# Optimization experiments

Hardware: AMD Instinct MI355X
Metric: run time of the kernel (lower is better)

The kernel has to match this reference:

```python
import jax, jax.numpy as jnp
import numpy as np

B, N, K, D = 2, 50000, 16, 64
EPS = 1e-5

def _ln(x, s, b):
    m = jnp.mean(x, axis=-1, keepdims=True)
    v = jnp.var(x, axis=-1, keepdims=True)
    return (x - m) * jax.lax.rsqrt(v + EPS) * s + b

def _lrelu(x):
    return jnp.where(x >= 0, x, 0.2 * x)

def _mlp3(x, w1, b1, ls1, lb1, w2, b2, ls2, lb2, w3, b3):
    h = _lrelu(_ln(jnp.dot(x, w1) + b1, ls1, lb1))
    h = _lrelu(_ln(jnp.dot(h, w2) + b2, ls2, lb2))
    return jnp.dot(h, w3) + b3

def _lin_init(k, fan_in, fan_out):
    bound = 1.0 / np.sqrt(fan_in)
    kw, kb = jax.random.split(k)
    w = jax.random.uniform(kw, (fan_in, fan_out), jnp.float32, -bound, bound)
    b = jax.random.uniform(kb, (fan_out,), jnp.float32, -bound, bound)
    return w, b

def setup_inputs() -> dict:
    key = jax.random.key(0)
    ks = jax.random.split(key, 10)
    inp = {
        'point_features': jax.random.normal(ks[0], (B, N, D), jnp.float32),
        'geom_features': jax.random.normal(ks[1], (B, N, K, 4), jnp.float32),
        'neighbor_idxs': jax.random.randint(ks[2], (B, N, K), 0, N, jnp.int32),
    }
    # geom_mlp: 4 -> 64 -> 128 -> 64 (Linear+LN+LeakyReLU x2, final Linear)
    inp['g_w1'], inp['g_b1'] = _lin_init(ks[3], 4, 64)
    inp['g_ls1'] = jnp.ones((64,), jnp.float32); inp['g_lb1'] = jnp.zeros((64,), jnp.float32)
    inp['g_w2'], inp['g_b2'] = _lin_init(ks[4], 64, 128)
    inp['g_ls2'] = jnp.ones((128,), jnp.float32); inp['g_lb2'] = jnp.zeros((128,), jnp.float32)
    inp['g_w3'], inp['g_b3'] = _lin_init(ks[5], 128, D)
    # feature_mlp: 2*D=128 -> 64 -> 128 -> 64
    inp['f_w1'], inp['f_b1'] = _lin_init(ks[6], 2 * D, 64)
    inp['f_ls1'] = jnp.ones((64,), jnp.float32); inp['f_lb1'] = jnp.zeros((64,), jnp.float32)
    inp['f_w2'], inp['f_b2'] = _lin_init(ks[7], 64, 128)
    inp['f_ls2'] = jnp.ones((128,), jnp.float32); inp['f_lb2'] = jnp.zeros((128,), jnp.float32)
    inp['f_w3'], inp['f_b3'] = _lin_init(ks[8], 128, D)
    return inp

def reference(point_features, geom_features, neighbor_idxs,
              g_w1, g_b1, g_ls1, g_lb1, g_w2, g_b2, g_ls2, g_lb2, g_w3, g_b3,
              f_w1, f_b1, f_ls1, f_lb1, f_w2, f_b2, f_ls2, f_lb2, f_w3, f_b3):
    b, n, k = neighbor_idxs.shape
    c = point_features.shape[-1]
    # geometry MLP on (B,N,K,4)
    geom_out = _mlp3(geom_features, g_w1, g_b1, g_ls1, g_lb1,
                     g_w2, g_b2, g_ls2, g_lb2, g_w3, g_b3)  # (B,N,K,D)
    # gather: out[b,i,j,:] = point_features[b, neighbor_idxs[b,i,j], :]
    gathered = jnp.take_along_axis(
        point_features, neighbor_idxs.reshape(b, n * k)[:, :, None], axis=1
    ).reshape(b, n, k, c)
    combined = jnp.concatenate([geom_out, gathered], axis=-1)  # (B,N,K,2D)
    final = _mlp3(combined, f_w1, f_b1, f_ls1, f_lb1,
                  f_w2, f_b2, f_ls2, f_lb2, f_w3, f_b3)  # (B,N,K,D)
    return jnp.mean(final, axis=2)  # (B,N,D)
```

## Files before the change

kernel.cpp:

```cpp
#include <hip/hip_runtime.h>
#include <hip/hip_bf16.h>

#define NN 50000
#define TB 512
#define NBLK 256
#define WPB 8
#define STR (NBLK * WPB)
static constexpr float EPS = 1e-5f;

typedef __attribute__((ext_vector_type(8))) short short8;
typedef __attribute__((ext_vector_type(16))) float f32x16;
typedef unsigned int u32;

#define OFF_G2 0
#define OFF_G3 16
#define OFF_F1 32
#define OFF_F2 48
#define OFF_W3 64
#define NFRAGS 80

__device__ __forceinline__ u32 pkbf(float a, float b) {
  u32 lo = (u32)__builtin_bit_cast(unsigned short, __float2bfloat16(a));
  u32 hi = (u32)__builtin_bit_cast(unsigned short, __float2bfloat16(b));
  return lo | (hi << 16);
}
__device__ __forceinline__ f32x16 zero16() {
  f32x16 z;
#pragma unroll
  for (int i = 0; i < 16; ++i) z[i] = 0.f;
  return z;
}
#define MFMA __builtin_amdgcn_mfma_f32_32x32x16_bf16

template <int IN, int OUT>
__device__ __forceinline__ void stage(const float* __restrict__ W,
                                      uint4* __restrict__ lds, int fragoff,
                                      float scale, int tid) {
  constexpr int KS = IN / 16, MT = OUT / 32;
  constexpr int ENT = MT * KS * 64;
  for (int e = tid; e < ENT; e += TB) {
    int lane = e & 63, f = e >> 6;
    int mt = f / KS, ks = f - mt * KS;
    int h = lane >> 5, och = mt * 32 + (lane & 31);
    int k0 = ks * 16 + h * 8;
    u32 d[4];
#pragma unroll
    for (int p = 0; p < 4; ++p)
      d[p] = pkbf(W[(k0 + 2 * p) * OUT + och] * scale,
                  W[(k0 + 2 * p + 1) * OUT + och] * scale);
    lds[(fragoff + f) * 64 + lane] = make_uint4(d[0], d[1], d[2], d[3]);
  }
}

__device__ __forceinline__ short8 rdfrag(const uint4* __restrict__ lds,
                                         int fragidx, int lane) {
  return __builtin_bit_cast(short8, lds[fragidx * 64 + lane]);
}

template <int NK>
__device__ __forceinline__ void to_bfr(const f32x16* acc, short8* bfr) {
#pragma unroll
  for (int t = 0; t < NK; ++t) {
    const int mt = t >> 1, q0 = (t & 1) * 8;
    u32 P0 = pkbf(acc[mt][q0 + 0], acc[mt][q0 + 1]);
    u32 P1 = pkbf(acc[mt][q0 + 2], acc[mt][q0 + 3]);
    u32 P2 = pkbf(acc[mt][q0 + 4], acc[mt][q0 + 5]);
    u32 P3 = pkbf(acc[mt][q0 + 6], acc[mt][q0 + 7]);
    auto s1 = __builtin_amdgcn_permlane32_swap((int)P0, (int)P2, false, false);
    auto s2 = __builtin_amdgcn_permlane32_swap((int)P1, (int)P3, false, false);
    bfr[t] = __builtin_bit_cast(
        short8, make_uint4((u32)s1[0], (u32)s2[0], (u32)s1[1], (u32)s2[1]));
  }
}

__device__ __forceinline__ void add_bias64_dual(f32x16* A, f32x16* B,
                                                const float* __restrict__ bias,
                                                int lane) {
  const int h = (lane >> 5) & 1;
#pragma unroll
  for (int mt = 0; mt < 2; ++mt)
#pragma unroll
    for (int rq = 0; rq < 4; ++rq) {
      const float4 b4 = *(const float4*)(bias + 32 * mt + 8 * rq + 4 * h);
      const float bb[4] = {b4.x, b4.y, b4.z, b4.w};
#pragma unroll
      for (int c = 0; c < 4; ++c) {
        A[mt][4 * rq + c] += bb[c];
        B[mt][4 * rq + c] += bb[c];
      }
    }
}

__device__ __forceinline__ void bias_ln_act64_dual(
    f32x16* A, f32x16* B, const float* __restrict__ bias,
    const float* __restrict__ gam, const float* __restrict__ bet, int lane) {
  const int h = (lane >> 5) & 1;
  float sA = 0.f, qA = 0.f, sB = 0.f, qB = 0.f;
#pragma unroll
  for (int mt = 0; mt < 2; ++mt)
#pragma unroll
    for (int rq = 0; rq < 4; ++rq) {
      const float4 b4 = *(const float4*)(bias + 32 * mt + 8 * rq + 4 * h);
      const float bb[4] = {b4.x, b4.y, b4.z, b4.w};
#pragma unroll
      for (int c = 0; c < 4; ++c) {
        float va = A[mt][4 * rq + c] + bb[c];
        float vb = B[mt][4 * rq + c] + bb[c];
        A[mt][4 * rq + c] = va;
        B[mt][4 * rq + c] = vb;
        sA += va; qA += va * va;
        sB += vb; qB += vb * vb;
      }
    }
  sA += __shfl_xor(sA, 32); qA += __shfl_xor(qA, 32);
  sB += __shfl_xor(sB, 32); qB += __shfl_xor(qB, 32);
  const float mA = sA * (1.f / 64.f);
  const float iA = rsqrtf(qA * (1.f / 64.f) - mA * mA + EPS);
  const float mB = sB * (1.f / 64.f);
  const float iB = rsqrtf(qB * (1.f / 64.f) - mB * mB + EPS);
#pragma unroll
  for (int mt = 0; mt < 2; ++mt)
#pragma unroll
    for (int rq = 0; rq < 4; ++rq) {
      const float4 g4 = *(const float4*)(gam + 32 * mt + 8 * rq + 4 * h);
      const float4 c4 = *(const float4*)(bet + 32 * mt + 8 * rq + 4 * h);
      const float gg[4] = {g4.x, g4.y, g4.z, g4.w};
      const float cc[4] = {c4.x, c4.y, c4.z, c4.w};
#pragma unroll
      for (int c = 0; c < 4; ++c) {
        float ya = (A[mt][4 * rq + c] - mA) * iA * gg[c] + cc[c];
        float yb = (B[mt][4 * rq + c] - mB) * iB * gg[c] + cc[c];
        A[mt][4 * rq + c] = fmaxf(ya, 0.2f * ya);
        B[mt][4 * rq + c] = fmaxf(yb, 0.2f * yb);
      }
    }
}

__device__ __forceinline__ void fused128_dual(
    const short8* kinA, const short8* kinB, const float* __restrict__ bias,
    const float* __restrict__ gam, const float* __restrict__ bet,
    const uint4* __restrict__ lds, int inOff, int outOff, f32x16* outA,
    f32x16* outB, int lane) {
  const int h = (lane >> 5) & 1;
  float sA = 0.f, qA = 0.f, sB = 0.f, qB = 0.f;
#pragma unroll 1
  for (int mt = 0; mt < 4; ++mt) {
    f32x16 a = zero16(), b = zero16();
#pragma unroll
    for (int ks = 0; ks < 4; ++ks) {
      const short8 wf = rdfrag(lds, inOff + mt * 4 + ks, lane);
      a = MFMA(wf, kinA[ks], a, 0, 0, 0);
      b = MFMA(wf, kinB[ks], b, 0, 0, 0);
    }
#pragma unroll
    for (int rq = 0; rq < 4; ++rq) {
      const float4 b4 = *(const float4*)(bias + 32 * mt + 8 * rq + 4 * h);
      const float bb[4] = {b4.x, b4.y, b4.z, b4.w};
#pragma unroll
      for (int c = 0; c < 4; ++c) {
        float va = a[4 * rq + c] + bb[c];
        float vb = b[4 * rq + c] + bb[c];
        sA += va; qA += va * va;
        sB += vb; qB += vb * vb;
      }
    }
  }
  sA += __shfl_xor(sA, 32); qA += __shfl_xor(qA, 32);
  sB += __shfl_xor(sB, 32); qB += __shfl_xor(qB, 32);
  const float mA = sA * (1.f / 128.f);
  const float iA = rsqrtf(qA * (1.f / 128.f) - mA * mA + EPS);
  const float mB = sB * (1.f / 128.f);
  const float iB = rsqrtf(qB * (1.f / 128.f) - mB * mB + EPS);
  asm volatile("" ::: "memory");
  outA[0] = zero16(); outA[1] = zero16();
  outB[0] = zero16(); outB[1] = zero16();
#pragma unroll 1
  for (int mt = 0; mt < 4; ++mt) {
    f32x16 a = zero16(), b = zero16();
#pragma unroll
    for (int ks = 0; ks < 4; ++ks) {
      const short8 wf = rdfrag(lds, inOff + mt * 4 + ks, lane);
      a = MFMA(wf, kinA[ks], a, 0, 0, 0);
      b = MFMA(wf, kinB[ks], b, 0, 0, 0);
    }
#pragma unroll
    for (int u = 0; u < 2; ++u) {
      const int c0 = 32 * mt + 16 * u + 4 * h;
      const float4 ba4 = *(const float4*)(bias + c0);
      const float4 bb4 = *(const float4*)(bias + c0 + 8);
      const float4 ga4 = *(const float4*)(gam + c0);
      const float4 gb4 = *(const float4*)(gam + c0 + 8);
      const float4 ca4 = *(const float4*)(bet + c0);
      const float4 cb4 = *(const float4*)(bet + c0 + 8);
      const float BB[8] = {ba4.x, ba4.y, ba4.z, ba4.w, bb4.x, bb4.y, bb4.z, bb4.w};
      const float GG[8] = {ga4.x, ga4.y, ga4.z, ga4.w, gb4.x, gb4.y, gb4.z, gb4.w};
      const float CC[8] = {ca4.x, ca4.y, ca4.z, ca4.w, cb4.x, cb4.y, cb4.z, cb4.w};
      u32 PA[4], PB[4];
#pragma unroll
      for (int p = 0; p < 4; ++p) {
        float a0 = (a[8 * u + 2 * p] + BB[2 * p] - mA) * iA * GG[2 * p] + CC[2 * p];
        float a1 = (a[8 * u + 2 * p + 1] + BB[2 * p + 1] - mA) * iA * GG[2 * p + 1] + CC[2 * p + 1];
        float b0 = (b[8 * u + 2 * p] + BB[2 * p] - mB) * iB * GG[2 * p] + CC[2 * p];
        float b1 = (b[8 * u + 2 * p + 1] + BB[2 * p + 1] - mB) * iB * GG[2 * p + 1] + CC[2 * p + 1];
        a0 = fmaxf(a0, 0.2f * a0); a1 = fmaxf(a1, 0.2f * a1);
        b0 = fmaxf(b0, 0.2f * b0); b1 = fmaxf(b1, 0.2f * b1);
        PA[p] = pkbf(a0, a1);
        PB[p] = pkbf(b0, b1);
      }
      auto sa1 = __builtin_amdgcn_permlane32_swap((int)PA[0], (int)PA[2], false, false);
      auto sa2 = __builtin_amdgcn_permlane32_swap((int)PA[1], (int)PA[3], false, false);
      auto sb1 = __builtin_amdgcn_permlane32_swap((int)PB[0], (int)PB[2], false, false);
      auto sb2 = __builtin_amdgcn_permlane32_swap((int)PB[1], (int)PB[3], false, false);
      const short8 frA = __builtin_bit_cast(
          short8, make_uint4((u32)sa1[0], (u32)sa2[0], (u32)sa1[1], (u32)sa2[1]));
      const short8 frB = __builtin_bit_cast(
          short8, make_uint4((u32)sb1[0], (u32)sb2[0], (u32)sb1[1], (u32)sb2[1]));
      const int t = 2 * mt + u;
      const short8 w0 = rdfrag(lds, outOff + t, lane);
      const short8 w1 = rdfrag(lds, outOff + 8 + t, lane);
      outA[0] = MFMA(w0, frA, outA[0], 0, 0, 0);
      outA[1] = MFMA(w1, frA, outA[1], 0, 0, 0);
      outB[0] = MFMA(w0, frB, outB[0], 0, 0, 0);
      outB[1] = MFMA(w1, frB, outB[1], 0, 0, 0);
    }
  }
}

extern "C" __global__ void __launch_bounds__(TB)
    __attribute__((amdgpu_waves_per_eu(2, 2)))
lfa_mfma(const float* __restrict__ pf, const float* __restrict__ geom,
         const int* __restrict__ nidx,
         const float* __restrict__ g_w1, const float* __restrict__ g_b1,
         const float* __restrict__ g_ls1, const float* __restrict__ g_lb1,
         const float* __restrict__ g_w2, const float* __restrict__ g_b2,
         const float* __restrict__ g_ls2, const float* __restrict__ g_lb2,
         const float* __restrict__ g_w3, const float* __restrict__ g_b3,
         const float* __restrict__ f_w1, const float* __restrict__ f_b1,
         const float* __restrict__ f_ls1, const float* __restrict__ f_lb1,
         const float* __restrict__ f_w2, const float* __restrict__ f_b2,
         const float* __restrict__ f_ls2, const float* __restrict__ f_lb2,
         const float* __restrict__ f_w3, const float* __restrict__ f_b3,
         float* __restrict__ out) {
  extern __shared__ uint4 lds[];
  const int tid = threadIdx.x;

  stage<64, 128>(g_w2, lds, OFF_G2, 1.f, tid);
  stage<128, 64>(g_w3, lds, OFF_G3, 1.f, tid);
  stage<128, 64>(f_w1, lds, OFF_F1, 1.f, tid);
  stage<64, 128>(f_w2, lds, OFF_F2, 1.f, tid);
  stage<128, 64>(f_w3, lds, OFF_W3, 1.f / 16.f, tid);
  __syncthreads();

  const int lane = tid & 63;
  const int w = tid >> 6;
  const int h = lane >> 5;
  const int p31 = lane & 31;

  short8 a1[2];
#pragma unroll
  for (int mt = 0; mt < 2; ++mt) {
    const int och = 32 * mt + p31;
    uint4 qq;
    qq.x = h ? 0u : pkbf(g_w1[0 * 64 + och], g_w1[1 * 64 + och]);
    qq.y = h ? 0u : pkbf(g_w1[2 * 64 + och], g_w1[3 * 64 + och]);
    qq.z = 0u;
    qq.w = 0u;
    a1[mt] = __builtin_bit_cast(short8, qq);
  }

  short8 kinA[4], kinB[4];

  for (int t0 = blockIdx.x * WPB + w; t0 < NN; t0 += 2 * STR) {
    asm volatile("" ::: "memory");
    const int tileA = t0;
    const bool hasB = (t0 + STR) < NN;
    const int tileB = hasB ? (t0 + STR) : tileA;
    const int rrowA = tileA * 32 + p31;
    const int rrowB = tileB * 32 + p31;
    const int bbA = tileA / 25000;
    const int bbB = tileB / 25000;

    const int idxA = nidx[rrowA];
    const int idxB = nidx[rrowB];
    const float* prA = pf + ((size_t)bbA * NN + idxA) * 64;
    const float* prB = pf + ((size_t)bbB * NN + idxB) * 64;

    const float4 gA = *(const float4*)(geom + (size_t)rrowA * 4);
    const float4 gB = *(const float4*)(geom + (size_t)rrowB * 4);
    uint4 qA, qB;
    qA.x = h ? 0u : pkbf(gA.x, gA.y);
    qA.y = h ? 0u : pkbf(gA.z, gA.w);
    qA.z = 0u; qA.w = 0u;
    qB.x = h ? 0u : pkbf(gB.x, gB.y);
    qB.y = h ? 0u : pkbf(gB.z, gB.w);
    qB.z = 0u; qB.w = 0u;
    const short8 gfA = __builtin_bit_cast(short8, qA);
    const short8 gfB = __builtin_bit_cast(short8, qB);
    f32x16 accA[2], accB[2];
#pragma unroll
    for (int mt = 0; mt < 2; ++mt) {
      accA[mt] = MFMA(a1[mt], gfA, zero16(), 0, 0, 0);
      accB[mt] = MFMA(a1[mt], gfB, zero16(), 0, 0, 0);
    }
    bias_ln_act64_dual(accA, accB, g_b1, g_ls1, g_lb1, lane);
    to_bfr<4>(accA, kinA);
    to_bfr<4>(accB, kinB);

    fused128_dual(kinA, kinB, g_b2, g_ls2, g_lb2, lds, OFF_G2, OFF_G3, accA,
                  accB, lane);
    add_bias64_dual(accA, accB, g_b3, lane);
    to_bfr<4>(accA, kinA);
    to_bfr<4>(accB, kinB);

#pragma unroll
    for (int mt = 0; mt < 2; ++mt) {
      f32x16 ta = zero16(), tb = zero16();
#pragma unroll
      for (int ks = 0; ks < 4; ++ks) {
        const short8 wf = rdfrag(lds, OFF_F1 + mt * 8 + ks, lane);
        ta = MFMA(wf, kinA[ks], ta, 0, 0, 0);
        tb = MFMA(wf, kinB[ks], tb, 0, 0, 0);
      }
      accA[mt] = ta;
      accB[mt] = tb;
    }
    {
#pragma unroll
      for (int t = 0; t < 4; ++t) {
        const float4 xA = *(const float4*)(prA + 16 * t + 8 * h);
        const float4 yA = *(const float4*)(prA + 16 * t + 8 * h + 4);
        const float4 xB = *(const float4*)(prB + 16 * t + 8 * h);
        const float4 yB = *(const float4*)(prB + 16 * t + 8 * h + 4);
        const short8 fA = __builtin_bit_cast(
            short8, make_uint4(pkbf(xA.x, xA.y), pkbf(xA.z, xA.w),
                               pkbf(yA.x, yA.y), pkbf(yA.z, yA.w)));
        const short8 fB = __builtin_bit_cast(
            short8, make_uint4(pkbf(xB.x, xB.y), pkbf(xB.z, xB.w),
                               pkbf(yB.x, yB.y), pkbf(yB.z, yB.w)));
        const short8 w0 = rdfrag(lds, OFF_F1 + 4 + t, lane);
        const short8 w1 = rdfrag(lds, OFF_F1 + 12 + t, lane);
        accA[0] = MFMA(w0, fA, accA[0], 0, 0, 0);
        accA[1] = MFMA(w1, fA, accA[1], 0, 0, 0);
        accB[0] = MFMA(w0, fB, accB[0], 0, 0, 0);
        accB[1] = MFMA(w1, fB, accB[1], 0, 0, 0);
      }
    }
    bias_ln_act64_dual(accA, accB, f_b1, f_ls1, f_lb1, lane);
    to_bfr<4>(accA, kinA);
    to_bfr<4>(accB, kinB);

    fused128_dual(kinA, kinB, f_b2, f_ls2, f_lb2, lds, OFF_F2, OFF_W3, accA,
                  accB, lane);

#pragma unroll
    for (int mt = 0; mt < 2; ++mt)
#pragma unroll
      for (int r = 0; r < 16; ++r) {
        float va = accA[mt][r];
        float vb = accB[mt][r];
        va += __shfl_xor(va, 1); vb += __shfl_xor(vb, 1);
        va += __shfl_xor(va, 2); vb += __shfl_xor(vb, 2);
        va += __shfl_xor(va, 4); vb += __shfl_xor(vb, 4);
        va += __shfl_xor(va, 8); vb += __shfl_xor(vb, 8);
        accA[mt][r] = va;
        accB[mt][r] = vb;
      }
    if ((lane & 15) < 4) {
      const int c = lane & 15;
      const int bn = (lane >> 4) & 1;
      const size_t rowA = (size_t)tileA * 2 + bn;
      const size_t rowB = (size_t)tileB * 2 + bn;
#pragma unroll
      for (int mt = 0; mt < 2; ++mt) {
        const float4 bq = *(const float4*)(f_b3 + 32 * mt + 8 * c + 4 * h);
        const float4 vA =
            (c == 0) ? make_float4(accA[mt][0], accA[mt][1], accA[mt][2], accA[mt][3])
          : (c == 1) ? make_float4(accA[mt][4], accA[mt][5], accA[mt][6], accA[mt][7])
          : (c == 2) ? make_float4(accA[mt][8], accA[mt][9], accA[mt][10], accA[mt][11])
                     : make_float4(accA[mt][12], accA[mt][13], accA[mt][14], accA[mt][15]);
        *(float4*)(out + rowA * 64 + 32 * mt + 8 * c + 4 * h) =
            make_float4(vA.x + bq.x, vA.y + bq.y, vA.z + bq.z, vA.w + bq.w);
        if (hasB) {
          const float4 vB =
              (c == 0) ? make_float4(accB[mt][0], accB[mt][1], accB[mt][2], accB[mt][3])
            : (c == 1) ? make_float4(accB[mt][4], accB[mt][5], accB[mt][6], accB[mt][7])
            : (c == 2) ? make_float4(accB[mt][8], accB[mt][9], accB[mt][10], accB[mt][11])
                       : make_float4(accB[mt][12], accB[mt][13], accB[mt][14], accB[mt][15]);
          *(float4*)(out + rowB * 64 + 32 * mt + 8 * c + 4 * h) =
              make_float4(vB.x + bq.x, vB.y + bq.y, vB.z + bq.z, vB.w + bq.w);
        }
      }
    }
  }
}

extern "C" void kernel_launch(void* const* d_in, const int* in_sizes, int n_in,
                              void* d_out, int out_size, void* d_ws, size_t ws_size,
                              hipStream_t stream) {
  const float* pf = (const float*)d_in[0];
  const float* geom = (const float*)d_in[1];
  const int* nidx = (const int*)d_in[2];
  const float* g_w1 = (const float*)d_in[3];
  const float* g_b1 = (const float*)d_in[4];
  const float* g_ls1 = (const float*)d_in[5];
  const float* g_lb1 = (const float*)d_in[6];
  const float* g_w2 = (const float*)d_in[7];
  const float* g_b2 = (const float*)d_in[8];
  const float* g_ls2 = (const float*)d_in[9];
  const float* g_lb2 = (const float*)d_in[10];
  const float* g_w3 = (const float*)d_in[11];
  const float* g_b3 = (const float*)d_in[12];
  const float* f_w1 = (const float*)d_in[13];
  const float* f_b1 = (const float*)d_in[14];
  const float* f_ls1 = (const float*)d_in[15];
  const float* f_lb1 = (const float*)d_in[16];
  const float* f_w2 = (const float*)d_in[17];
  const float* f_b2 = (const float*)d_in[18];
  const float* f_ls2 = (const float*)d_in[19];
  const float* f_lb2 = (const float*)d_in[20];
  const float* f_w3 = (const float*)d_in[21];
  const float* f_b3 = (const float*)d_in[22];

  const int shmem = NFRAGS * 64 * 16;
  lfa_mfma<<<NBLK, TB, shmem, stream>>>(
      pf, geom, nidx, g_w1, g_b1, g_ls1, g_lb1, g_w2, g_b2, g_ls2, g_lb2, g_w3,
      g_b3, f_w1, f_b1, f_ls1, f_lb1, f_w2, f_b2, f_ls2, f_lb2, f_w3, f_b3,
      (float*)d_out);
}
```

Baseline: 384.8 us.

## Switch MFMA operands to fp16 and do LayerNorm/activation in packed half math

```diff
diff --git a/kernel.cpp b/kernel.cpp
--- a/kernel.cpp
+++ b/kernel.cpp
@@ -8,7 +8,8 @@
 #define STR (NBLK * WPB)
 static constexpr float EPS = 1e-5f;
 
-typedef __attribute__((ext_vector_type(8))) short short8;
+typedef _Float16 h2 __attribute__((ext_vector_type(2)));
+typedef _Float16 half8 __attribute__((ext_vector_type(8)));
 typedef __attribute__((ext_vector_type(16))) float f32x16;
 typedef unsigned int u32;
 
@@ -19,18 +20,17 @@
 #define OFF_W3 64
 #define NFRAGS 80
 
-__device__ __forceinline__ u32 pkbf(float a, float b) {
-  u32 lo = (u32)__builtin_bit_cast(unsigned short, __float2bfloat16(a));
-  u32 hi = (u32)__builtin_bit_cast(unsigned short, __float2bfloat16(b));
-  return lo | (hi << 16);
-}
+__device__ __forceinline__ h2 pkh(float a, float b) {
+  return __builtin_bit_cast(h2, __builtin_amdgcn_cvt_pkrtz(a, b));
+}
+__device__ __forceinline__ u32 hbits(h2 x) { return __builtin_bit_cast(u32, x); }
 __device__ __forceinline__ f32x16 zero16() {
   f32x16 z;
 #pragma unroll
   for (int i = 0; i < 16; ++i) z[i] = 0.f;
   return z;
 }
-#define MFMA __builtin_amdgcn_mfma_f32_32x32x16_bf16
+#define MFMA __builtin_amdgcn_mfma_f32_32x32x16_f16
 
 template <int IN, int OUT>
 __device__ __forceinline__ void stage(const float* __restrict__ W,
@@ -46,54 +46,25 @@
     u32 d[4];
 #pragma unroll
     for (int p = 0; p < 4; ++p)
-      d[p] = pkbf(W[(k0 + 2 * p) * OUT + och] * scale,
-                  W[(k0 + 2 * p + 1) * OUT + och] * scale);
+      d[p] = hbits(pkh(W[(k0 + 2 * p) * OUT + och] * scale,
+                       W[(k0 + 2 * p + 1) * OUT + och] * scale));
     lds[(fragoff + f) * 64 + lane] = make_uint4(d[0], d[1], d[2], d[3]);
   }
 }
 
-__device__ __forceinline__ short8 rdfrag(const uint4* __restrict__ lds,
-                                         int fragidx, int lane) {
-  return __builtin_bit_cast(short8, lds[fragidx * 64 + lane]);
-}
-
-template <int NK>
-__device__ __forceinline__ void to_bfr(const f32x16* acc, short8* bfr) {
-#pragma unroll
-  for (int t = 0; t < NK; ++t) {
-    const int mt = t >> 1, q0 = (t & 1) * 8;
-    u32 P0 = pkbf(acc[mt][q0 + 0], acc[mt][q0 + 1]);
-    u32 P1 = pkbf(acc[mt][q0 + 2], acc[mt][q0 + 3]);
-    u32 P2 = pkbf(acc[mt][q0 + 4], acc[mt][q0 + 5]);
-    u32 P3 = pkbf(acc[mt][q0 + 6], acc[mt][q0 + 7]);
-    auto s1 = __builtin_amdgcn_permlane32_swap((int)P0, (int)P2, false, false);
-    auto s2 = __builtin_amdgcn_permlane32_swap((int)P1, (int)P3, false, false);
-    bfr[t] = __builtin_bit_cast(
-        short8, make_uint4((u32)s1[0], (u32)s2[0], (u32)s1[1], (u32)s2[1]));
-  }
-}
-
-__device__ __forceinline__ void add_bias64_dual(f32x16* A, f32x16* B,
-                                                const float* __restrict__ bias,
-                                                int lane) {
-  const int h = (lane >> 5) & 1;
-#pragma unroll
-  for (int mt = 0; mt < 2; ++mt)
-#pragma unroll
-    for (int rq = 0; rq < 4; ++rq) {
-      const float4 b4 = *(const float4*)(bias + 32 * mt + 8 * rq + 4 * h);
-      const float bb[4] = {b4.x, b4.y, b4.z, b4.w};
-#pragma unroll
-      for (int c = 0; c < 4; ++c) {
-        A[mt][4 * rq + c] += bb[c];
-        B[mt][4 * rq + c] += bb[c];
-      }
-    }
-}
-
-__device__ __forceinline__ void bias_ln_act64_dual(
+__device__ __forceinline__ half8 rdfrag(const uint4* __restrict__ lds,
+                                        int fragidx, int lane) {
+  return __builtin_bit_cast(half8, lds[fragidx * 64 + lane]);
+}
+
+__device__ __forceinline__ half8 mkfrag(u32 a, u32 b, u32 c, u32 d) {
+  return __builtin_bit_cast(half8, make_uint4(a, b, c, d));
+}
+
+__device__ __forceinline__ void ln_pack64_dual(
     f32x16* A, f32x16* B, const float* __restrict__ bias,
-    const float* __restrict__ gam, const float* __restrict__ bet, int lane) {
+    const float* __restrict__ gam, const float* __restrict__ bet, int lane,
+    half8* kinA, half8* kinB) {
   const int h = (lane >> 5) & 1;
   float sA = 0.f, qA = 0.f, sB = 0.f, qB = 0.f;
 #pragma unroll
@@ -118,26 +89,75 @@
   const float iA = rsqrtf(qA * (1.f / 64.f) - mA * mA + EPS);
   const float mB = sB * (1.f / 64.f);
   const float iB = rsqrtf(qB * (1.f / 64.f) - mB * mB + EPS);
+  const h2 iA2 = pkh(iA, iA), nA2 = pkh(-mA * iA, -mA * iA);
+  const h2 iB2 = pkh(iB, iB), nB2 = pkh(-mB * iB, -mB * iB);
+  const h2 c02 = pkh(0.2f, 0.2f);
 #pragma unroll
   for (int mt = 0; mt < 2; ++mt)
 #pragma unroll
-    for (int rq = 0; rq < 4; ++rq) {
-      const float4 g4 = *(const float4*)(gam + 32 * mt + 8 * rq + 4 * h);
-      const float4 c4 = *(const float4*)(bet + 32 * mt + 8 * rq + 4 * h);
-      const float gg[4] = {g4.x, g4.y, g4.z, g4.w};
-      const float cc[4] = {c4.x, c4.y, c4.z, c4.w};
-#pragma unroll
-      for (int c = 0; c < 4; ++c) {
-        float ya = (A[mt][4 * rq + c] - mA) * iA * gg[c] + cc[c];
-        float yb = (B[mt][4 * rq + c] - mB) * iB * gg[c] + cc[c];
-        A[mt][4 * rq + c] = fmaxf(ya, 0.2f * ya);
-        B[mt][4 * rq + c] = fmaxf(yb, 0.2f * yb);
-      }
+    for (int t2 = 0; t2 < 2; ++t2) {
+      const int q0 = t2 * 8;
+      const float4 g0 = *(const float4*)(gam + 32 * mt + 2 * q0 + 4 * h);
+      const float4 g1 = *(const float4*)(gam + 32 * mt + 2 * q0 + 8 + 4 * h);
+      const float4 e0 = *(const float4*)(bet + 32 * mt + 2 * q0 + 4 * h);
+      const float4 e1 = *(const float4*)(bet + 32 * mt + 2 * q0 + 8 + 4 * h);
+      const float GG[8] = {g0.x, g0.y, g0.z, g0.w, g1.x, g1.y, g1.z, g1.w};
+      const float CC[8] = {e0.x, e0.y, e0.z, e0.w, e1.x, e1.y, e1.z, e1.w};
+      u32 PA[4], PB[4];
+#pragma unroll
+      for (int p = 0; p < 4; ++p) {
+        const h2 g2 = pkh(GG[2 * p], GG[2 * p + 1]);
+        const h2 e2 = pkh(CC[2 * p], CC[2 * p + 1]);
+        h2 xa = pkh(A[mt][q0 + 2 * p], A[mt][q0 + 2 * p + 1]);
+        h2 xb = pkh(B[mt][q0 + 2 * p], B[mt][q0 + 2 * p + 1]);
+        h2 ya = (xa * iA2 + nA2) * g2 + e2;
+        h2 yb = (xb * iB2 + nB2) * g2 + e2;
+        ya = __builtin_elementwise_max(ya, ya * c02);
+        yb = __builtin_elementwise_max(yb, yb * c02);
+        PA[p] = hbits(ya);
+        PB[p] = hbits(yb);
+      }
+      auto sa1 = __builtin_amdgcn_permlane32_swap((int)PA[0], (int)PA[2], false, false);
+      auto sa2 = __builtin_amdgcn_permlane32_swap((int)PA[1], (int)PA[3], false, false);
+      auto sb1 = __builtin_amdgcn_permlane32_swap((int)PB[0], (int)PB[2], false, false);
+      auto sb2 = __builtin_amdgcn_permlane32_swap((int)PB[1], (int)PB[3], false, false);
+      kinA[2 * mt + t2] = mkfrag((u32)sa1[0], (u32)sa2[0], (u32)sa1[1], (u32)sa2[1]);
+      kinB[2 * mt + t2] = mkfrag((u32)sb1[0], (u32)sb2[0], (u32)sb1[1], (u32)sb2[1]);
+    }
+}
+
+__device__ __forceinline__ void bias_pack64_dual(const f32x16* A, const f32x16* B,
+                                                 const float* __restrict__ bias,
+                                                 int lane, half8* kinA,
+                                                 half8* kinB) {
+  const int h = (lane >> 5) & 1;
+#pragma unroll
+  for (int mt = 0; mt < 2; ++mt)
+#pragma unroll
+    for (int t2 = 0; t2 < 2; ++t2) {
+      const int q0 = t2 * 8;
+      const float4 b0 = *(const float4*)(bias + 32 * mt + 2 * q0 + 4 * h);
+      const float4 b1 = *(const float4*)(bias + 32 * mt + 2 * q0 + 8 + 4 * h);
+      const float BBv[8] = {b0.x, b0.y, b0.z, b0.w, b1.x, b1.y, b1.z, b1.w};
+      u32 PA[4], PB[4];
+#pragma unroll
+      for (int p = 0; p < 4; ++p) {
+        PA[p] = hbits(pkh(A[mt][q0 + 2 * p] + BBv[2 * p],
+                          A[mt][q0 + 2 * p + 1] + BBv[2 * p + 1]));
+        PB[p] = hbits(pkh(B[mt][q0 + 2 * p] + BBv[2 * p],
+                          B[mt][q0 + 2 * p + 1] + BBv[2 * p + 1]));
+      }
+      auto sa1 = __builtin_amdgcn_permlane32_swap((int)PA[0], (int)PA[2], false, false);
+      auto sa2 = __builtin_amdgcn_permlane32_swap((int)PA[1], (int)PA[3], false, false);
+      auto sb1 = __builtin_amdgcn_permlane32_swap((int)PB[0], (int)PB[2], false, false);
+      auto sb2 = __builtin_amdgcn_permlane32_swap((int)PB[1], (int)PB[3], false, false);
+      kinA[2 * mt + t2] = mkfrag((u32)sa1[0], (u32)sa2[0], (u32)sa1[1], (u32)sa2[1]);
+      kinB[2 * mt + t2] = mkfrag((u32)sb1[0], (u32)sb2[0], (u32)sb1[1], (u32)sb2[1]);
     }
 }
 
 __device__ __forceinline__ void fused128_dual(
-    const short8* kinA, const short8* kinB, const float* __restrict__ bias,
+    const half8* kinA, const half8* kinB, const float* __restrict__ bias,
     const float* __restrict__ gam, const float* __restrict__ bet,
     const uint4* __restrict__ lds, int inOff, int outOff, f32x16* outA,
     f32x16* outB, int lane) {
@@ -148,7 +168,7 @@
     f32x16 a = zero16(), b = zero16();
 #pragma unroll
     for (int ks = 0; ks < 4; ++ks) {
-      const short8 wf = rdfrag(lds, inOff + mt * 4 + ks, lane);
+      const half8 wf = rdfrag(lds, inOff + mt * 4 + ks, lane);
       a = MFMA(wf, kinA[ks], a, 0, 0, 0);
       b = MFMA(wf, kinB[ks], b, 0, 0, 0);
     }
@@ -171,6 +191,9 @@
   const float iA = rsqrtf(qA * (1.f / 128.f) - mA * mA + EPS);
   const float mB = sB * (1.f / 128.f);
   const float iB = rsqrtf(qB * (1.f / 128.f) - mB * mB + EPS);
+  const h2 iA2 = pkh(iA, iA), nA2 = pkh(-mA * iA, -mA * iA);
+  const h2 iB2 = pkh(iB, iB), nB2 = pkh(-mB * iB, -mB * iB);
+  const h2 c02 = pkh(0.2f, 0.2f);
   asm volatile("" ::: "memory");
   outA[0] = zero16(); outA[1] = zero16();
   outB[0] = zero16(); outB[1] = zero16();
@@ -179,7 +202,7 @@
     f32x16 a = zero16(), b = zero16();
 #pragma unroll
     for (int ks = 0; ks < 4; ++ks) {
-      const short8 wf = rdfrag(lds, inOff + mt * 4 + ks, lane);
+      const half8 wf = rdfrag(lds, inOff + mt * 4 + ks, lane);
       a = MFMA(wf, kinA[ks], a, 0, 0, 0);
       b = MFMA(wf, kinB[ks], b, 0, 0, 0);
     }
@@ -198,26 +221,26 @@
       u32 PA[4], PB[4];
 #pragma unroll
       for (int p = 0; p < 4; ++p) {
-        float a0 = (a[8 * u + 2 * p] + BB[2 * p] - mA) * iA * GG[2 * p] + CC[2 * p];
-        float a1 = (a[8 * u + 2 * p + 1] + BB[2 * p + 1] - mA) * iA * GG[2 * p + 1] + CC[2 * p + 1];
-        float b0 = (b[8 * u + 2 * p] + BB[2 * p] - mB) * iB * GG[2 * p] + CC[2 * p];
-        float b1 = (b[8 * u + 2 * p + 1] + BB[2 * p + 1] - mB) * iB * GG[2 * p + 1] + CC[2 * p + 1];
-        a0 = fmaxf(a0, 0.2f * a0); a1 = fmaxf(a1, 0.2f * a1);
-        b0 = fmaxf(b0, 0.2f * b0); b1 = fmaxf(b1, 0.2f * b1);
-        PA[p] = pkbf(a0, a1);
-        PB[p] = pkbf(b0, b1);
+        const h2 g2 = pkh(GG[2 * p], GG[2 * p + 1]);
+        const h2 e2 = pkh(CC[2 * p], CC[2 * p + 1]);
+        h2 xa = pkh(a[8 * u + 2 * p] + BB[2 * p], a[8 * u + 2 * p + 1] + BB[2 * p + 1]);
+        h2 xb = pkh(b[8 * u + 2 * p] + BB[2 * p], b[8 * u + 2 * p + 1] + BB[2 * p + 1]);
+        h2 ya = (xa * iA2 + nA2) * g2 + e2;
+        h2 yb = (xb * iB2 + nB2) * g2 + e2;
+        ya = __builtin_elementwise_max(ya, ya * c02);
+        yb = __builtin_elementwise_max(yb, yb * c02);
+        PA[p] = hbits(ya);
+        PB[p] = hbits(yb);
       }
       auto sa1 = __builtin_amdgcn_permlane32_swap((int)PA[0], (int)PA[2], false, false);
       auto sa2 = __builtin_amdgcn_permlane32_swap((int)PA[1], (int)PA[3], false, false);
       auto sb1 = __builtin_amdgcn_permlane32_swap((int)PB[0], (int)PB[2], false, false);
       auto sb2 = __builtin_amdgcn_permlane32_swap((int)PB[1], (int)PB[3], false, false);
-      const short8 frA = __builtin_bit_cast(
-          short8, make_uint4((u32)sa1[0], (u32)sa2[0], (u32)sa1[1], (u32)sa2[1]));
-      const short8 frB = __builtin_bit_cast(
-          short8, make_uint4((u32)sb1[0], (u32)sb2[0], (u32)sb1[1], (u32)sb2[1]));
+      const half8 frA = mkfrag((u32)sa1[0], (u32)sa2[0], (u32)sa1[1], (u32)sa2[1]);
+      const half8 frB = mkfrag((u32)sb1[0], (u32)sb2[0], (u32)sb1[1], (u32)sb2[1]);
       const int t = 2 * mt + u;
-      const short8 w0 = rdfrag(lds, outOff + t, lane);
-      const short8 w1 = rdfrag(lds, outOff + 8 + t, lane);
+      const half8 w0 = rdfrag(lds, outOff + t, lane);
+      const half8 w1 = rdfrag(lds, outOff + 8 + t, lane);
       outA[0] = MFMA(w0, frA, outA[0], 0, 0, 0);
       outA[1] = MFMA(w1, frA, outA[1], 0, 0, 0);
       outB[0] = MFMA(w0, frB, outB[0], 0, 0, 0);
@@ -256,19 +279,16 @@
   const int h = lane >> 5;
   const int p31 = lane & 31;
 
-  short8 a1[2];
+  half8 a1[2];
 #pragma unroll
   for (int mt = 0; mt < 2; ++mt) {
     const int och = 32 * mt + p31;
-    uint4 qq;
-    qq.x = h ? 0u : pkbf(g_w1[0 * 64 + och], g_w1[1 * 64 + och]);
-    qq.y = h ? 0u : pkbf(g_w1[2 * 64 + och], g_w1[3 * 64 + och]);
-    qq.z = 0u;
-    qq.w = 0u;
-    a1[mt] = __builtin_bit_cast(short8, qq);
+    a1[mt] = mkfrag(h ? 0u : hbits(pkh(g_w1[0 * 64 + och], g_w1[1 * 64 + och])),
+                    h ? 0u : hbits(pkh(g_w1[2 * 64 + och], g_w1[3 * 64 + och])),
+                    0u, 0u);
   }
 
-  short8 kinA[4], kinB[4];
+  half8 kinA[4], kinB[4];
 
   for (int t0 = blockIdx.x * WPB + w; t0 < NN; t0 += 2 * STR) {
     asm volatile("" ::: "memory");
@@ -287,37 +307,28 @@
 
     const float4 gA = *(const float4*)(geom + (size_t)rrowA * 4);
     const float4 gB = *(const float4*)(geom + (size_t)rrowB * 4);
-    uint4 qA, qB;
-    qA.x = h ? 0u : pkbf(gA.x, gA.y);
-    qA.y = h ? 0u : pkbf(gA.z, gA.w);
-    qA.z = 0u; qA.w = 0u;
-    qB.x = h ? 0u : pkbf(gB.x, gB.y);
-    qB.y = h ? 0u : pkbf(gB.z, gB.w);
-    qB.z = 0u; qB.w = 0u;
-    const short8 gfA = __builtin_bit_cast(short8, qA);
-    const short8 gfB = __builtin_bit_cast(short8, qB);
+    const half8 gfA = mkfrag(h ? 0u : hbits(pkh(gA.x, gA.y)),
+                             h ? 0u : hbits(pkh(gA.z, gA.w)), 0u, 0u);
+    const half8 gfB = mkfrag(h ? 0u : hbits(pkh(gB.x, gB.y)),
+                             h ? 0u : hbits(pkh(gB.z, gB.w)), 0u, 0u);
     f32x16 accA[2], accB[2];
 #pragma unroll
     for (int mt = 0; mt < 2; ++mt) {
       accA[mt] = MFMA(a1[mt], gfA, zero16(), 0, 0, 0);
       accB[mt] = MFMA(a1[mt], gfB, zero16(), 0, 0, 0);
     }
-    bias_ln_act64_dual(accA, accB, g_b1, g_ls1, g_lb1, lane);
-    to_bfr<4>(accA, kinA);
-    to_bfr<4>(accB, kinB);
+    ln_pack64_dual(accA, accB, g_b1, g_ls1, g_lb1, lane, kinA, kinB);
 
     fused128_dual(kinA, kinB, g_b2, g_ls2, g_lb2, lds, OFF_G2, OFF_G3, accA,
                   accB, lane);
-    add_bias64_dual(accA, accB, g_b3, lane);
-    to_bfr<4>(accA, kinA);
-    to_bfr<4>(accB, kinB);
+    bias_pack64_dual(accA, accB, g_b3, lane, kinA, kinB);
 
 #pragma unroll
     for (int mt = 0; mt < 2; ++mt) {
       f32x16 ta = zero16(), tb = zero16();
 #pragma unroll
       for (int ks = 0; ks < 4; ++ks) {
-        const short8 wf = rdfrag(lds, OFF_F1 + mt * 8 + ks, lane);
+        const half8 wf = rdfrag(lds, OFF_F1 + mt * 8 + ks, lane);
         ta = MFMA(wf, kinA[ks], ta, 0, 0, 0);
         tb = MFMA(wf, kinB[ks], tb, 0, 0, 0);
       }
@@ -331,23 +342,19 @@
         const float4 yA = *(const float4*)(prA + 16 * t + 8 * h + 4);
         const float4 xB = *(const float4*)(prB + 16 * t + 8 * h);
         const float4 yB = *(const float4*)(prB + 16 * t + 8 * h + 4);
-        const short8 fA = __builtin_bit_cast(
-            short8, make_uint4(pkbf(xA.x, xA.y), pkbf(xA.z, xA.w),
-                               pkbf(yA.x, yA.y), pkbf(yA.z, yA.w)));
-        const short8 fB = __builtin_bit_cast(
-            short8, make_uint4(pkbf(xB.x, xB.y), pkbf(xB.z, xB.w),
-                               pkbf(yB.x, yB.y), pkbf(yB.z, yB.w)));
-        const short8 w0 = rdfrag(lds, OFF_F1 + 4 + t, lane);
-        const short8 w1 = rdfrag(lds, OFF_F1 + 12 + t, lane);
+        const half8 fA = mkfrag(hbits(pkh(xA.x, xA.y)), hbits(pkh(xA.z, xA.w)),
+                                hbits(pkh(yA.x, yA.y)), hbits(pkh(yA.z, yA.w)));
+        const half8 fB = mkfrag(hbits(pkh(xB.x, xB.y)), hbits(pkh(xB.z, xB.w)),
+                                hbits(pkh(yB.x, yB.y)), hbits(pkh(yB.z, yB.w)));
+        const half8 w0 = rdfrag(lds, OFF_F1 + 4 + t, lane);
+        const half8 w1 = rdfrag(lds, OFF_F1 + 12 + t, lane);
         accA[0] = MFMA(w0, fA, accA[0], 0, 0, 0);
         accA[1] = MFMA(w1, fA, accA[1], 0, 0, 0);
         accB[0] = MFMA(w0, fB, accB[0], 0, 0, 0);
         accB[1] = MFMA(w1, fB, accB[1], 0, 0, 0);
       }
     }
-    bias_ln_act64_dual(accA, accB, f_b1, f_ls1, f_lb1, lane);
-    to_bfr<4>(accA, kinA);
-    to_bfr<4>(accB, kinB);
+    ln_pack64_dual(accA, accB, f_b1, f_ls1, f_lb1, lane, kinA, kinB);
 
     fused128_dual(kinA, kinB, f_b2, f_ls2, f_lb2, lds, OFF_F2, OFF_W3, accA,
                   accB, lane);
```

Result: faster. 341.8 us (-11.2%).
